# Kernel optimization log

Measured on AMD Instinct MI355X. Metric: run time of the kernel, lower is better.

Reference implementation:

```python
import jax, jax.numpy as jnp
import numpy as np

B, L, Z, G = 512, 2713, 58, 8  # batch, chem features, seq len (zeta), d_model (gamma)
H, HD, FF, NL = 8, 1, 2048, 6  # heads, head_dim, ffn dim, layers
RNA_IN, LIN1, LIN2 = 1018, 256, 64
CAT, C1, C2 = LIN2 + Z * G, 64, 8  # 528, 64, 8


def setup_inputs() -> dict:
    key = jax.random.key(0)
    ks = iter(jax.random.split(key, 40))
    r = lambda shape, s=0.05: (jax.random.normal(next(ks), shape, dtype=jnp.float32) * s)
    inp = {
        'rna': jax.random.normal(next(ks), (B, RNA_IN), dtype=jnp.float32),
        'drug': jax.random.normal(next(ks), (B, L, Z), dtype=jnp.float32),
        'lin1_w': r((LIN1, RNA_IN)), 'lin1_b': r((LIN1,)),
        'lin2_w': r((LIN2, LIN1)), 'lin2_b': r((LIN2,)),
        'chem_w': r((G, L)),  # chem_embedding: Linear(2713->8, no bias)
        'pos_w': r((G, Z)),   # pos_embedding on one-hot == its weight columns
        'qkv_w': r((NL, 3 * G, G)), 'qkv_b': r((NL, 3 * G)),
        'out_w': r((NL, G, G)), 'out_b': r((NL, G)),
        'ln1_g': jnp.ones((NL, G), jnp.float32), 'ln1_b': jnp.zeros((NL, G), jnp.float32),
        'ff1_w': r((NL, FF, G)), 'ff1_b': r((NL, FF)),
        'ff2_w': r((NL, G, FF)), 'ff2_b': r((NL, G)),
        'ln2_g': jnp.ones((NL, G), jnp.float32), 'ln2_b': jnp.zeros((NL, G), jnp.float32),
        'c1_w': r((C1, CAT)), 'c1_b': r((C1,)),
        'c2_w': r((C2, C1)), 'c2_b': r((C2,)),
        'c3_w': r((1, C2)), 'c3_b': r((1,)),
    }
    return inp


def _layernorm(x, g, b, eps=1e-5):
    mu = jnp.mean(x, axis=-1, keepdims=True)
    var = jnp.mean(jnp.square(x - mu), axis=-1, keepdims=True)
    return (x - mu) * jax.lax.rsqrt(var + eps) * g + b


def _forward(rna, drug, lin1_w, lin1_b, lin2_w, lin2_b, chem_w, pos_w,
             qkv_w, qkv_b, out_w, out_b, ln1_g, ln1_b,
             ff1_w, ff1_b, ff2_w, ff2_b, ln2_g, ln2_b,
             c1_w, c1_b, c2_w, c2_b, c3_w, c3_b):
    # rna branch: two linear layers (no activation in original forward)
    r = rna @ lin1_w.T + lin1_b
    r = r @ lin2_w.T + lin2_b  # [B, 64]

    # Embedding: E = W_chem @ M + W_pos (the double loop, vectorized)
    E = jnp.einsum('gl,blz->bgz', chem_w, drug) + pos_w[None]  # [B, G, Z]
    x = jnp.transpose(E, (0, 2, 1))  # [B, Z, G] (batch_first transformer input)

    scale = 1.0 / np.sqrt(HD)
    for i in range(NL):  # 6 post-norm TransformerEncoderLayers, relu FFN
        qkv = x @ qkv_w[i].T + qkv_b[i]  # [B, Z, 3G]
        q, k, v = jnp.split(qkv, 3, axis=-1)
        qh = q.reshape(B, Z, H, HD)
        kh = k.reshape(B, Z, H, HD)
        vh = v.reshape(B, Z, H, HD)
        scores = jnp.einsum('bshd,bthd->bhst', qh, kh) * scale
        a = jax.nn.softmax(scores, axis=-1)
        o = jnp.einsum('bhst,bthd->bshd', a, vh).reshape(B, Z, G)
        o = o @ out_w[i].T + out_b[i]
        x = _layernorm(x + o, ln1_g[i], ln1_b[i])
        ff = jax.nn.relu(x @ ff1_w[i].T + ff1_b[i]) @ ff2_w[i].T + ff2_b[i]
        x = _layernorm(x + ff, ln2_g[i], ln2_b[i])

    flat = x.reshape(B, Z * G)  # [B, 464]
    h = jnp.concatenate([r, flat], axis=1)  # [B, 528]
    h = h @ c1_w.T + c1_b
    h = h @ c2_w.T + c2_b
    return h @ c3_w.T + c3_b  # [B, 1]


def reference(rna, drug, lin1_w, lin1_b, lin2_w, lin2_b, chem_w, pos_w,
              qkv_w, qkv_b, out_w, out_b, ln1_g, ln1_b,
              ff1_w, ff1_b, ff2_w, ff2_b, ln2_g, ln2_b,
              c1_w, c1_b, c2_w, c2_b, c3_w, c3_b):
    return _forward(rna, drug, lin1_w, lin1_b, lin2_w, lin2_b, chem_w, pos_w,
                    qkv_w, qkv_b, out_w, out_b, ln1_g, ln1_b,
                    ff1_w, ff1_b, ff2_w, ff2_b, ln2_g, ln2_b,
                    c1_w, c1_b, c2_w, c2_b, c3_w, c3_b)
```

## Files before the change

### kernel.cpp

```cpp
#include <hip/hip_runtime.h>

#define BB 512
#define LDIM 2713
#define ZDIM 58
#define GDIM 8
#define NLAYER 6
#define FFDIM 2048
#define RNAIN 1018
#define CATDIM 528
#define NCAT 1482
#define LQ 679

typedef float v2f __attribute__((ext_vector_type(2)));
typedef float f32x4 __attribute__((ext_vector_type(4)));
typedef _Float16 f16x4 __attribute__((ext_vector_type(4)));

#define OFF_WCATT  0
#define OFF_BPRIME 94848

__global__ __launch_bounds__(1024) void prep_kernel(
    const float* __restrict__ lin1_w, const float* __restrict__ lin1_b,
    const float* __restrict__ lin2_w, const float* __restrict__ lin2_b,
    const float* __restrict__ c1_w, const float* __restrict__ c1_b,
    float* __restrict__ ws) {
    __shared__ float lin1s[256 * 64];
    __shared__ float Ut[64 * 64];
    __shared__ float c1T[64 * 64];
    const int t = threadIdx.x;
    float* WcatT = ws + OFF_WCATT;

    if (blockIdx.x == 16) {
        {
            int m = t >> 4, q = t & 15;
            float a = 0.f;
            #pragma unroll
            for (int nn = 0; nn < 16; ++nn)
                a += lin2_w[m * 256 + q * 16 + nn] * lin1_b[q * 16 + nn];
            lin1s[m * 16 + q] = a;
        }
        __syncthreads();
        if (t < 64) {
            float a = lin2_b[t];
            #pragma unroll
            for (int q = 0; q < 16; ++q) a += lin1s[t * 16 + q];
            Ut[t] = a;
        }
        __syncthreads();
        if (t < 64) {
            float a = c1_b[t];
            #pragma unroll 8
            for (int m = 0; m < 64; ++m) a += c1_w[t * CATDIM + m] * Ut[m];
            ws[OFF_BPRIME + t] = a;
        }
        for (int i = t; i < 464 * 64; i += 1024) {
            int j = i / 464, kk = i % 464;
            WcatT[(RNAIN + kk) * 64 + j] = c1_w[j * CATDIM + 64 + kk];
        }
        return;
    }

    const int k0 = blockIdx.x * 64;
    const int nk = (RNAIN - k0 < 64) ? (RNAIN - k0) : 64;
    for (int i = t; i < 256 * 64; i += 1024) {
        int n = i >> 6, kl = i & 63;
        lin1s[i] = (kl < nk) ? lin1_w[n * RNAIN + k0 + kl] : 0.f;
    }
    for (int i = t; i < 64 * 64; i += 1024) {
        int j = i >> 6, m = i & 63;
        c1T[m * 64 + j] = c1_w[j * CATDIM + m];
    }
    __syncthreads();
    for (int mp = 0; mp < 4; ++mp) {
        int m = (t >> 6) + mp * 16;
        int kl = t & 63;
        const float* l2r = lin2_w + m * 256;
        float a = 0.f;
        #pragma unroll 8
        for (int n = 0; n < 256; ++n) a += l2r[n] * lin1s[n * 64 + kl];
        Ut[m * 64 + kl] = a;
    }
    __syncthreads();
    for (int kp = 0; kp < 4; ++kp) {
        int kr = (t >> 6) + kp * 16;
        int j = t & 63;
        if (kr < nk) {
            float a = 0.f;
            #pragma unroll 8
            for (int m = 0; m < 64; ++m) a += Ut[m * 64 + kr] * c1T[m * 64 + j];
            WcatT[(k0 + kr) * 64 + j] = a;
        }
    }
}

__global__ __launch_bounds__(512, 8) void mega_kernel(
    const float* __restrict__ drug, const float* __restrict__ chem_w,
    const float* __restrict__ pos_w,
    const float* __restrict__ ff1_w, const float* __restrict__ ff2_w,
    const float* __restrict__ ff1_b,
    const float* __restrict__ qkv_w, const float* __restrict__ qkv_b,
    const float* __restrict__ out_w, const float* __restrict__ out_b,
    const float* __restrict__ ln1_g, const float* __restrict__ ln1_b,
    const float* __restrict__ ff2_b,
    const float* __restrict__ ln2_g, const float* __restrict__ ln2_b,
    const float* __restrict__ rna, const float* __restrict__ WcatT,
    const float* __restrict__ bprime,
    const float* __restrict__ c2_w, const float* __restrict__ c2_b,
    const float* __restrict__ c3_w, const float* __restrict__ c3_b,
    float* __restrict__ out) {
    __shared__ float smem[9152];
    float* cwl    = smem;
    float* part_e = smem + 5440;
    float* xs    = smem;
    float* qs    = smem + 512;
    float* ks    = smem + 992;
    float* vs    = smem + 1472;
    float* part  = smem + 1952;
    float* qkvws = smem + 6048;
    float* qkvbs = smem + 7200;
    float* outws = smem + 7344;
    float* outbs = smem + 7728;
    float* l1gs  = smem + 7776;
    float* l1bs  = smem + 7824;
    float* l2gs  = smem + 7872;
    float* l2bs  = smem + 7920;
    float* f2bs  = smem + 7968;
    float* h1s   = smem + 8016;
    float* h2s   = smem + 8080;

    const int b = blockIdx.x;
    const int t = threadIdx.x;
    const int w = __builtin_amdgcn_readfirstlane(t >> 6);
    const int lane = t & 63;
    const int quad = lane >> 4;
    const int i16 = lane & 15;

    {
        const int zc = (lane < ZDIM) ? lane : (ZDIM - 1);
        v2f acc0 = {0.f, 0.f}, acc1 = {0.f, 0.f}, acc2 = {0.f, 0.f}, acc3 = {0.f, 0.f};
        for (int q = 0; q < 4; ++q) {
            const int l0 = q * LQ;
            const int nrows = (LDIM - l0 < LQ) ? (LDIM - l0) : LQ;
            __syncthreads();
            #pragma unroll
            for (int g = 0; g < 8; ++g)
                for (int i = t; i < nrows; i += 512)
                    cwl[i * 8 + g] = chem_w[g * LDIM + l0 + i];
            __syncthreads();
            const float* dp = drug + (size_t)b * (LDIM * ZDIM) + (size_t)l0 * ZDIM;
            int r0 = w * 85;
            int r1 = (r0 + 85 < nrows) ? (r0 + 85) : nrows;
            int r = r0;
            for (; r + 4 <= r1; r += 4) {
                float d0 = dp[(r + 0) * ZDIM + zc];
                float d1 = dp[(r + 1) * ZDIM + zc];
                float d2 = dp[(r + 2) * ZDIM + zc];
                float d3 = dp[(r + 3) * ZDIM + zc];
                const v2f* c0 = (const v2f*)(cwl + (r + 0) * 8);
                const v2f* c1 = (const v2f*)(cwl + (r + 1) * 8);
                const v2f* c2 = (const v2f*)(cwl + (r + 2) * 8);
                const v2f* c3 = (const v2f*)(cwl + (r + 3) * 8);
                v2f dd;
                dd = (v2f){d0, d0};
                acc0 += c0[0] * dd; acc1 += c0[1] * dd; acc2 += c0[2] * dd; acc3 += c0[3] * dd;
                dd = (v2f){d1, d1};
                acc0 += c1[0] * dd; acc1 += c1[1] * dd; acc2 += c1[2] * dd; acc3 += c1[3] * dd;
                dd = (v2f){d2, d2};
                acc0 += c2[0] * dd; acc1 += c2[1] * dd; acc2 += c2[2] * dd; acc3 += c2[3] * dd;
                dd = (v2f){d3, d3};
                acc0 += c3[0] * dd; acc1 += c3[1] * dd; acc2 += c3[2] * dd; acc3 += c3[3] * dd;
            }
            for (; r < r1; ++r) {
                float d = dp[r * ZDIM + zc];
                const v2f* cc = (const v2f*)(cwl + r * 8);
                v2f dd = {d, d};
                acc0 += cc[0] * dd; acc1 += cc[1] * dd; acc2 += cc[2] * dd; acc3 += cc[3] * dd;
            }
        }
        if (lane < ZDIM) {
            v2f* pr = (v2f*)(part_e + w * 464 + zc * 8);
            pr[0] = acc0; pr[1] = acc1; pr[2] = acc2; pr[3] = acc3;
        }
        __syncthreads();
        if (t < 464) {
            int z = t >> 3, g = t & 7;
            float s = pos_w[g * ZDIM + z];
            #pragma unroll
            for (int ww = 0; ww < 8; ++ww) s += part_e[ww * 464 + t];
            xs[t] = s;
        } else if (t < 512) {
            xs[t] = 0.f;
        }
        __syncthreads();
    }

    for (int i = t; i < 1152; i += 512) qkvws[i] = qkv_w[i];
    if (t < 144) qkvbs[t] = qkv_b[t];
    if (t < 384) outws[t] = out_w[t];
    if (t < 48) {
        outbs[t] = out_b[t];
        l1gs[t] = ln1_g[t]; l1bs[t] = ln1_b[t];
        l2gs[t] = ln2_g[t]; l2bs[t] = ln2_b[t];
        f2bs[t] = ff2_b[t];
    }
    __syncthreads();

    for (int li = 0; li < NLAYER; ++li) {
        if (t < 464) {
            int z = t >> 3, h = t & 7;
            const float4* xr = (const float4*)(xs + z * 8);
            float4 x0 = xr[0], x1 = xr[1];
            #pragma unroll
            for (int p = 0; p < 3; ++p) {
                int j = p * 8 + h;
                const float4* wr = (const float4*)(qkvws + li * 192 + j * 8);
                float4 w0 = wr[0], w1 = wr[1];
                float a = qkvbs[li * 24 + j]
                        + x0.x * w0.x + x0.y * w0.y + x0.z * w0.z + x0.w * w0.w
                        + x1.x * w1.x + x1.y * w1.y + x1.z * w1.z + x1.w * w1.w;
                float* dst = (p == 0) ? qs : (p == 1) ? ks : vs;
                dst[h * 60 + z] = a;
            }
        }
        __syncthreads();

        if (t < 464) {
            int h = t & 7, s = t >> 3;
            float q = qs[h * 60 + s];
            const float4* kr = (const float4*)(ks + h * 60);
            const float4* vr = (const float4*)(vs + h * 60);
            float sum = 0.f, oa = 0.f;
            #pragma unroll 2
            for (int c = 0; c < 14; ++c) {
                float4 k4 = kr[c], v4 = vr[c];
                float e0 = __expf(q * k4.x); sum += e0; oa += e0 * v4.x;
                float e1 = __expf(q * k4.y); sum += e1; oa += e1 * v4.y;
                float e2 = __expf(q * k4.z); sum += e2; oa += e2 * v4.z;
                float e3 = __expf(q * k4.w); sum += e3; oa += e3 * v4.w;
            }
            {
                const float* kk = ks + h * 60;
                const float* vv = vs + h * 60;
                float e0 = __expf(q * kk[56]); sum += e0; oa += e0 * vv[56];
                float e1 = __expf(q * kk[57]); sum += e1; oa += e1 * vv[57];
            }
            float o = oa / sum;
            int g = h;
            float a = outbs[li * 8 + g] + xs[t];
            const float* wr8 = outws + li * 64 + g * 8;
            #pragma unroll
            for (int hh = 0; hh < 8; ++hh)
                a += __shfl(o, hh, 8) * wr8[hh];
            float s8 = a + __shfl_xor(a, 1);
            s8 += __shfl_xor(s8, 2);
            s8 += __shfl_xor(s8, 4);
            float mu = s8 * 0.125f;
            float d = a - mu;
            float vv = d * d;
            vv += __shfl_xor(vv, 1); vv += __shfl_xor(vv, 2); vv += __shfl_xor(vv, 4);
            float inv = rsqrtf(vv * 0.125f + 1e-5f);
            xs[t] = d * inv * l1gs[li * 8 + g] + l1bs[li * 8 + g];
        }
        __syncthreads();

        {
            f16x4 xb[4];
            #pragma unroll
            for (int nt = 0; nt < 4; ++nt) {
                if (quad < 2) {
                    const float4* xp = (const float4*)(xs + (nt * 16 + i16) * 8 + quad * 4);
                    float4 xv = *xp;
                    xb[nt][0] = (_Float16)xv.x; xb[nt][1] = (_Float16)xv.y;
                    xb[nt][2] = (_Float16)xv.z; xb[nt][3] = (_Float16)xv.w;
                } else {
                    xb[nt][0] = (_Float16)0.f; xb[nt][1] = (_Float16)0.f;
                    xb[nt][2] = (_Float16)0.f; xb[nt][3] = (_Float16)0.f;
                }
            }
            f32x4 oacc[4];
            #pragma unroll
            for (int nt = 0; nt < 4; ++nt) { oacc[nt][0]=0.f; oacc[nt][1]=0.f; oacc[nt][2]=0.f; oacc[nt][3]=0.f; }

            const float* w1p = ff1_w + ((size_t)li * FFDIM + w * 256) * 8;
            const float* a2p = ff2_w + (size_t)li * GDIM * FFDIM + w * 256;
            const float* b1p = ff1_b + li * FFDIM + w * 256;

            #pragma unroll 2
            for (int ft = 0; ft < 16; ++ft) {
                f16x4 w1f = {};
                if (lane < 32) {
                    f32x4 v = *(const f32x4*)(w1p + (size_t)(ft * 16 + i16) * 8 + quad * 4);
                    w1f[0] = (_Float16)v[0]; w1f[1] = (_Float16)v[1];
                    w1f[2] = (_Float16)v[2]; w1f[3] = (_Float16)v[3];
                }
                f16x4 a2f = {};
                if (i16 < 8) {
                    f32x4 v = *(const f32x4*)(a2p + (size_t)i16 * FFDIM + ft * 16 + quad * 4);
                    a2f[0] = (_Float16)v[0]; a2f[1] = (_Float16)v[1];
                    a2f[2] = (_Float16)v[2]; a2f[3] = (_Float16)v[3];
                }
                f32x4 b1v = *(const f32x4*)(b1p + ft * 16 + quad * 4);
                #pragma unroll
                for (int nt = 0; nt < 4; ++nt) {
                    f32x4 h = b1v;
                    h = __builtin_amdgcn_mfma_f32_16x16x16f16(w1f, xb[nt], h, 0, 0, 0);
                    h[0] = fmaxf(h[0], 0.f); h[1] = fmaxf(h[1], 0.f);
                    h[2] = fmaxf(h[2], 0.f); h[3] = fmaxf(h[3], 0.f);
                    f16x4 hb;
                    hb[0] = (_Float16)h[0]; hb[1] = (_Float16)h[1];
                    hb[2] = (_Float16)h[2]; hb[3] = (_Float16)h[3];
                    oacc[nt] = __builtin_amdgcn_mfma_f32_16x16x16f16(a2f, hb, oacc[nt], 0, 0, 0);
                }
            }
            if (quad < 2) {
                #pragma unroll
                for (int nt = 0; nt < 4; ++nt) {
                    float4 o4 = make_float4(oacc[nt][0], oacc[nt][1], oacc[nt][2], oacc[nt][3]);
                    *(float4*)(part + ((w * 64 + nt * 16 + i16) * 8 + quad * 4)) = o4;
                }
            }
        }
        __syncthreads();

        if (t < 464) {
            int z = t >> 3, g = t & 7;
            float s = 0.f;
            #pragma unroll
            for (int ww = 0; ww < 8; ++ww) s += part[(ww * 64 + z) * 8 + g];
            float a = xs[t] + s + f2bs[li * 8 + g];
            float s8 = a + __shfl_xor(a, 1);
            s8 += __shfl_xor(s8, 2);
            s8 += __shfl_xor(s8, 4);
            float mu = s8 * 0.125f;
            float d = a - mu;
            float vv = d * d;
            vv += __shfl_xor(vv, 1); vv += __shfl_xor(vv, 2); vv += __shfl_xor(vv, 4);
            float inv = rsqrtf(vv * 0.125f + 1e-5f);
            xs[t] = d * inv * l2gs[li * 8 + g] + l2bs[li * 8 + g];
        }
        __syncthreads();
    }

    {
        float* cat = part;
        float* partial = part + 1024;
        const float* rg = rna + (size_t)b * RNAIN;
        for (int i = t; i < RNAIN; i += 512) cat[i] = rg[i];
        __syncthreads();
        int j = lane;
        int k0 = w * 186;
        int k1 = (k0 + 186 < NCAT) ? (k0 + 186) : NCAT;
        float a = (w == 0) ? bprime[j] : 0.f;
        #pragma unroll 4
        for (int k = k0; k < k1; ++k) {
            float ck = (k < RNAIN) ? cat[k] : xs[k - RNAIN];
            a += ck * WcatT[k * 64 + j];
        }
        partial[w * 64 + j] = a;
        __syncthreads();
        if (t < 64) {
            float s = 0.f;
            #pragma unroll
            for (int ww = 0; ww < 8; ++ww) s += partial[ww * 64 + t];
            h1s[t] = s;
        }
    }
    __syncthreads();
    if (t < 8) {
        float a2 = c2_b[t];
        #pragma unroll 8
        for (int m = 0; m < 64; ++m) a2 += h1s[m] * c2_w[t * 64 + m];
        h2s[t] = a2;
    }
    __syncthreads();
    if (t == 0) {
        float a3 = c3_b[0];
        #pragma unroll
        for (int jj = 0; jj < 8; ++jj) a3 += h2s[jj] * c3_w[jj];
        out[b] = a3;
    }
}

extern "C" void kernel_launch(void* const* d_in, const int* in_sizes, int n_in,
                              void* d_out, int out_size, void* d_ws, size_t ws_size,
                              hipStream_t stream) {
    const float* rna    = (const float*)d_in[0];
    const float* drug   = (const float*)d_in[1];
    const float* lin1_w = (const float*)d_in[2];
    const float* lin1_b = (const float*)d_in[3];
    const float* lin2_w = (const float*)d_in[4];
    const float* lin2_b = (const float*)d_in[5];
    const float* chem_w = (const float*)d_in[6];
    const float* pos_w  = (const float*)d_in[7];
    const float* qkv_w  = (const float*)d_in[8];
    const float* qkv_b  = (const float*)d_in[9];
    const float* out_w  = (const float*)d_in[10];
    const float* out_b  = (const float*)d_in[11];
    const float* ln1_g  = (const float*)d_in[12];
    const float* ln1_b  = (const float*)d_in[13];
    const float* ff1_w  = (const float*)d_in[14];
    const float* ff1_b  = (const float*)d_in[15];
    const float* ff2_w  = (const float*)d_in[16];
    const float* ff2_b  = (const float*)d_in[17];
    const float* ln2_g  = (const float*)d_in[18];
    const float* ln2_b  = (const float*)d_in[19];
    const float* c1_w   = (const float*)d_in[20];
    const float* c1_b   = (const float*)d_in[21];
    const float* c2_w   = (const float*)d_in[22];
    const float* c2_b   = (const float*)d_in[23];
    const float* c3_w   = (const float*)d_in[24];
    const float* c3_b   = (const float*)d_in[25];
    float* ws  = (float*)d_ws;
    float* out = (float*)d_out;

    hipLaunchKernelGGL(prep_kernel, dim3(17), dim3(1024), 0, stream,
                       lin1_w, lin1_b, lin2_w, lin2_b, c1_w, c1_b, ws);
    hipLaunchKernelGGL(mega_kernel, dim3(BB), dim3(512), 0, stream,
                       drug, chem_w, pos_w, ff1_w, ff2_w, ff1_b,
                       qkv_w, qkv_b, out_w, out_b,
                       ln1_g, ln1_b, ff2_b, ln2_g, ln2_b,
                       rna, ws + OFF_WCATT, ws + OFF_BPRIME,
                       c2_w, c2_b, c3_w, c3_b, out);
}
```

Before: 698.9 us.

## Double mega_kernel block size, pre-pack FFN weights to fp16, restructure prep GEMMs

Measured after the change: 650.7 us. -6.9%, faster.

```diff
diff --git a/kernel.cpp b/kernel.cpp
--- a/kernel.cpp
+++ b/kernel.cpp
@@ -17,19 +17,49 @@
 
 #define OFF_WCATT  0
 #define OFF_BPRIME 94848
+#define OFF_W1H    94912
+#define OFF_A2H    144064
 
 __global__ __launch_bounds__(1024) void prep_kernel(
     const float* __restrict__ lin1_w, const float* __restrict__ lin1_b,
     const float* __restrict__ lin2_w, const float* __restrict__ lin2_b,
     const float* __restrict__ c1_w, const float* __restrict__ c1_b,
+    const float* __restrict__ ff1_w, const float* __restrict__ ff2_w,
     float* __restrict__ ws) {
+    const int t = threadIdx.x;
+    const int bx = blockIdx.x;
+    float* WcatT = ws + OFF_WCATT;
+
+    if (bx >= 17) {
+        int tid = (bx - 17) * 1024 + t;
+        _Float16* w1hp = (_Float16*)(ws + OFF_W1H);
+        _Float16* a2hp = (_Float16*)(ws + OFF_A2H);
+        if (tid < NLAYER * 128 * 32) {
+            int li = tid / 4096, rem = tid % 4096;
+            int ft = rem >> 5, l32 = rem & 31;
+            int q = l32 >> 4, i = l32 & 15;
+            const float* src = ff1_w + ((size_t)li * FFDIM + ft * 16 + i) * 8 + q * 4;
+            size_t dst = ((size_t)(li * 128 + ft) * 32 + l32) * 4;
+            #pragma unroll
+            for (int j = 0; j < 4; ++j) w1hp[dst + j] = (_Float16)src[j];
+        } else {
+            int r2 = tid - NLAYER * 128 * 32;
+            int li = r2 / 4096, rem = r2 % 4096;
+            int ft = rem >> 5, s = rem & 31;
+            int q = s >> 3, i2 = s & 7;
+            const float* src = ff2_w + ((size_t)li * GDIM + i2) * FFDIM + ft * 16 + q * 4;
+            size_t dst = ((size_t)(li * 128 + ft) * 32 + s) * 4;
+            #pragma unroll
+            for (int j = 0; j < 4; ++j) a2hp[dst + j] = (_Float16)src[j];
+        }
+        return;
+    }
+
     __shared__ float lin1s[256 * 64];
     __shared__ float Ut[64 * 64];
     __shared__ float c1T[64 * 64];
-    const int t = threadIdx.x;
-    float* WcatT = ws + OFF_WCATT;
-
-    if (blockIdx.x == 16) {
+
+    if (bx == 16) {
         {
             int m = t >> 4, q = t & 15;
             float a = 0.f;
@@ -59,7 +89,7 @@
         return;
     }
 
-    const int k0 = blockIdx.x * 64;
+    const int k0 = bx * 64;
     const int nk = (RNAIN - k0 < 64) ? (RNAIN - k0) : 64;
     for (int i = t; i < 256 * 64; i += 1024) {
         int n = i >> 6, kl = i & 63;
@@ -70,32 +100,45 @@
         c1T[m * 64 + j] = c1_w[j * CATDIM + m];
     }
     __syncthreads();
-    for (int mp = 0; mp < 4; ++mp) {
-        int m = (t >> 6) + mp * 16;
-        int kl = t & 63;
-        const float* l2r = lin2_w + m * 256;
-        float a = 0.f;
-        #pragma unroll 8
-        for (int n = 0; n < 256; ++n) a += l2r[n] * lin1s[n * 64 + kl];
-        Ut[m * 64 + kl] = a;
+    {
+        const int kl = t & 63;
+        const int mw = __builtin_amdgcn_readfirstlane(t >> 6);
+        float a0 = 0.f, a1 = 0.f, a2 = 0.f, a3 = 0.f;
+        for (int n = 0; n < 256; ++n) {
+            float ls = lin1s[n * 64 + kl];
+            a0 += lin2_w[(mw +  0) * 256 + n] * ls;
+            a1 += lin2_w[(mw + 16) * 256 + n] * ls;
+            a2 += lin2_w[(mw + 32) * 256 + n] * ls;
+            a3 += lin2_w[(mw + 48) * 256 + n] * ls;
+        }
+        Ut[(mw +  0) * 64 + kl] = a0;
+        Ut[(mw + 16) * 64 + kl] = a1;
+        Ut[(mw + 32) * 64 + kl] = a2;
+        Ut[(mw + 48) * 64 + kl] = a3;
     }
     __syncthreads();
-    for (int kp = 0; kp < 4; ++kp) {
-        int kr = (t >> 6) + kp * 16;
-        int j = t & 63;
-        if (kr < nk) {
-            float a = 0.f;
-            #pragma unroll 8
-            for (int m = 0; m < 64; ++m) a += Ut[m * 64 + kr] * c1T[m * 64 + j];
-            WcatT[(k0 + kr) * 64 + j] = a;
-        }
+    {
+        const int j = t & 63;
+        const int kw = __builtin_amdgcn_readfirstlane(t >> 6);
+        float a0 = 0.f, a1 = 0.f, a2 = 0.f, a3 = 0.f;
+        for (int m = 0; m < 64; ++m) {
+            float cv = c1T[m * 64 + j];
+            a0 += Ut[m * 64 + kw +  0] * cv;
+            a1 += Ut[m * 64 + kw + 16] * cv;
+            a2 += Ut[m * 64 + kw + 32] * cv;
+            a3 += Ut[m * 64 + kw + 48] * cv;
+        }
+        if (kw +  0 < nk) WcatT[(k0 + kw +  0) * 64 + j] = a0;
+        if (kw + 16 < nk) WcatT[(k0 + kw + 16) * 64 + j] = a1;
+        if (kw + 32 < nk) WcatT[(k0 + kw + 32) * 64 + j] = a2;
+        if (kw + 48 < nk) WcatT[(k0 + kw + 48) * 64 + j] = a3;
     }
 }
 
-__global__ __launch_bounds__(512, 8) void mega_kernel(
+__global__ __launch_bounds__(1024, 8) void mega_kernel(
     const float* __restrict__ drug, const float* __restrict__ chem_w,
     const float* __restrict__ pos_w,
-    const float* __restrict__ ff1_w, const float* __restrict__ ff2_w,
+    const _Float16* __restrict__ w1h, const _Float16* __restrict__ a2h,
     const float* __restrict__ ff1_b,
     const float* __restrict__ qkv_w, const float* __restrict__ qkv_b,
     const float* __restrict__ out_w, const float* __restrict__ out_b,
@@ -107,25 +150,26 @@
     const float* __restrict__ c2_w, const float* __restrict__ c2_b,
     const float* __restrict__ c3_w, const float* __restrict__ c3_b,
     float* __restrict__ out) {
-    __shared__ float smem[9152];
+    __shared__ float smem[12864];
     float* cwl    = smem;
     float* part_e = smem + 5440;
     float* xs    = smem;
-    float* qs    = smem + 512;
-    float* ks    = smem + 992;
-    float* vs    = smem + 1472;
-    float* part  = smem + 1952;
-    float* qkvws = smem + 6048;
-    float* qkvbs = smem + 7200;
-    float* outws = smem + 7344;
-    float* outbs = smem + 7728;
-    float* l1gs  = smem + 7776;
-    float* l1bs  = smem + 7824;
-    float* l2gs  = smem + 7872;
-    float* l2bs  = smem + 7920;
-    float* f2bs  = smem + 7968;
-    float* h1s   = smem + 8016;
-    float* h2s   = smem + 8080;
+    _Float16* xh = (_Float16*)(smem + 512);
+    float* qs    = smem + 768;
+    float* ks    = smem + 1248;
+    float* vs    = smem + 1728;
+    float* part  = smem + 2208;
+    float* qkvws = smem + 10400;
+    float* qkvbs = smem + 11552;
+    float* outws = smem + 11696;
+    float* outbs = smem + 12080;
+    float* l1gs  = smem + 12128;
+    float* l1bs  = smem + 12176;
+    float* l2gs  = smem + 12224;
+    float* l2bs  = smem + 12272;
+    float* f2bs  = smem + 12320;
+    float* h1s   = smem + 12368;
+    float* h2s   = smem + 12432;
 
     const int b = blockIdx.x;
     const int t = threadIdx.x;
@@ -142,38 +186,45 @@
             const int nrows = (LDIM - l0 < LQ) ? (LDIM - l0) : LQ;
             __syncthreads();
             #pragma unroll
-            for (int g = 0; g < 8; ++g)
-                for (int i = t; i < nrows; i += 512)
-                    cwl[i * 8 + g] = chem_w[g * LDIM + l0 + i];
+            for (int gp = 0; gp < 4; ++gp)
+                for (int i = t; i < nrows; i += 1024) {
+                    v2f cv = { chem_w[(2 * gp) * LDIM + l0 + i],
+                               chem_w[(2 * gp + 1) * LDIM + l0 + i] };
+                    *(v2f*)(cwl + 2 * (gp * 680 + i)) = cv;
+                }
             __syncthreads();
-            const float* dp = drug + (size_t)b * (LDIM * ZDIM) + (size_t)l0 * ZDIM;
-            int r0 = w * 85;
-            int r1 = (r0 + 85 < nrows) ? (r0 + 85) : nrows;
+            const float* dp = drug + (size_t)b * (LDIM * ZDIM) + (size_t)l0 * ZDIM + zc;
+            int r0 = w * 43;
+            int r1 = (r0 + 43 < nrows) ? (r0 + 43) : nrows;
             int r = r0;
-            for (; r + 4 <= r1; r += 4) {
-                float d0 = dp[(r + 0) * ZDIM + zc];
-                float d1 = dp[(r + 1) * ZDIM + zc];
-                float d2 = dp[(r + 2) * ZDIM + zc];
-                float d3 = dp[(r + 3) * ZDIM + zc];
-                const v2f* c0 = (const v2f*)(cwl + (r + 0) * 8);
-                const v2f* c1 = (const v2f*)(cwl + (r + 1) * 8);
-                const v2f* c2 = (const v2f*)(cwl + (r + 2) * 8);
-                const v2f* c3 = (const v2f*)(cwl + (r + 3) * 8);
-                v2f dd;
-                dd = (v2f){d0, d0};
-                acc0 += c0[0] * dd; acc1 += c0[1] * dd; acc2 += c0[2] * dd; acc3 += c0[3] * dd;
-                dd = (v2f){d1, d1};
-                acc0 += c1[0] * dd; acc1 += c1[1] * dd; acc2 += c1[2] * dd; acc3 += c1[3] * dd;
-                dd = (v2f){d2, d2};
-                acc0 += c2[0] * dd; acc1 += c2[1] * dd; acc2 += c2[2] * dd; acc3 += c2[3] * dd;
-                dd = (v2f){d3, d3};
-                acc0 += c3[0] * dd; acc1 += c3[1] * dd; acc2 += c3[2] * dd; acc3 += c3[3] * dd;
+            for (; r + 8 <= r1; r += 8) {
+                float d0 = dp[(r + 0) * ZDIM];
+                float d1 = dp[(r + 1) * ZDIM];
+                float d2 = dp[(r + 2) * ZDIM];
+                float d3 = dp[(r + 3) * ZDIM];
+                float d4 = dp[(r + 4) * ZDIM];
+                float d5 = dp[(r + 5) * ZDIM];
+                float d6 = dp[(r + 6) * ZDIM];
+                float d7 = dp[(r + 7) * ZDIM];
+                #pragma unroll
+                for (int j = 0; j < 8; ++j) {
+                    float dj = (j == 0) ? d0 : (j == 1) ? d1 : (j == 2) ? d2 : (j == 3) ? d3
+                             : (j == 4) ? d4 : (j == 5) ? d5 : (j == 6) ? d6 : d7;
+                    v2f dd = {dj, dj};
+                    int rr = r + j;
+                    acc0 += *(const v2f*)(cwl + 2 * (0 * 680 + rr)) * dd;
+                    acc1 += *(const v2f*)(cwl + 2 * (1 * 680 + rr)) * dd;
+                    acc2 += *(const v2f*)(cwl + 2 * (2 * 680 + rr)) * dd;
+                    acc3 += *(const v2f*)(cwl + 2 * (3 * 680 + rr)) * dd;
+                }
             }
             for (; r < r1; ++r) {
-                float d = dp[r * ZDIM + zc];
-                const v2f* cc = (const v2f*)(cwl + r * 8);
+                float d = dp[r * ZDIM];
                 v2f dd = {d, d};
-                acc0 += cc[0] * dd; acc1 += cc[1] * dd; acc2 += cc[2] * dd; acc3 += cc[3] * dd;
+                acc0 += *(const v2f*)(cwl + 2 * (0 * 680 + r)) * dd;
+                acc1 += *(const v2f*)(cwl + 2 * (1 * 680 + r)) * dd;
+                acc2 += *(const v2f*)(cwl + 2 * (2 * 680 + r)) * dd;
+                acc3 += *(const v2f*)(cwl + 2 * (3 * 680 + r)) * dd;
             }
         }
         if (lane < ZDIM) {
@@ -185,15 +236,16 @@
             int z = t >> 3, g = t & 7;
             float s = pos_w[g * ZDIM + z];
             #pragma unroll
-            for (int ww = 0; ww < 8; ++ww) s += part_e[ww * 464 + t];
+            for (int ww = 0; ww < 16; ++ww) s += part_e[ww * 464 + t];
             xs[t] = s;
         } else if (t < 512) {
             xs[t] = 0.f;
-        }
-        __syncthreads();
-    }
-
-    for (int i = t; i < 1152; i += 512) qkvws[i] = qkv_w[i];
+            xh[t] = (_Float16)0.f;
+        }
+        __syncthreads();
+    }
+
+    for (int i = t; i < 1152; i += 1024) qkvws[i] = qkv_w[i];
     if (t < 144) qkvbs[t] = qkv_b[t];
     if (t < 384) outws[t] = out_w[t];
     if (t < 48) {
@@ -205,21 +257,18 @@
     __syncthreads();
 
     for (int li = 0; li < NLAYER; ++li) {
-        if (t < 464) {
-            int z = t >> 3, h = t & 7;
+        for (int i = t; i < 1392; i += 1024) {
+            int z = i / 24, j = i - z * 24;
             const float4* xr = (const float4*)(xs + z * 8);
             float4 x0 = xr[0], x1 = xr[1];
-            #pragma unroll
-            for (int p = 0; p < 3; ++p) {
-                int j = p * 8 + h;
-                const float4* wr = (const float4*)(qkvws + li * 192 + j * 8);
-                float4 w0 = wr[0], w1 = wr[1];
-                float a = qkvbs[li * 24 + j]
-                        + x0.x * w0.x + x0.y * w0.y + x0.z * w0.z + x0.w * w0.w
-                        + x1.x * w1.x + x1.y * w1.y + x1.z * w1.z + x1.w * w1.w;
-                float* dst = (p == 0) ? qs : (p == 1) ? ks : vs;
-                dst[h * 60 + z] = a;
-            }
+            const float4* wr = (const float4*)(qkvws + li * 192 + j * 8);
+            float4 w0 = wr[0], w1 = wr[1];
+            float a = qkvbs[li * 24 + j]
+                    + x0.x * w0.x + x0.y * w0.y + x0.z * w0.z + x0.w * w0.w
+                    + x1.x * w1.x + x1.y * w1.y + x1.z * w1.z + x1.w * w1.w;
+            int p = j >> 3, h = j & 7;
+            float* dst = (p == 0) ? qs : (p == 1) ? ks : vs;
+            dst[h * 60 + z] = a;
         }
         __syncthreads();
 
@@ -258,7 +307,9 @@
             float vv = d * d;
             vv += __shfl_xor(vv, 1); vv += __shfl_xor(vv, 2); vv += __shfl_xor(vv, 4);
             float inv = rsqrtf(vv * 0.125f + 1e-5f);
-            xs[t] = d * inv * l1gs[li * 8 + g] + l1bs[li * 8 + g];
+            float xn = d * inv * l1gs[li * 8 + g] + l1bs[li * 8 + g];
+            xs[t] = xn;
+            xh[t] = (_Float16)xn;
         }
         __syncthreads();
 
@@ -267,10 +318,7 @@
             #pragma unroll
             for (int nt = 0; nt < 4; ++nt) {
                 if (quad < 2) {
-                    const float4* xp = (const float4*)(xs + (nt * 16 + i16) * 8 + quad * 4);
-                    float4 xv = *xp;
-                    xb[nt][0] = (_Float16)xv.x; xb[nt][1] = (_Float16)xv.y;
-                    xb[nt][2] = (_Float16)xv.z; xb[nt][3] = (_Float16)xv.w;
+                    xb[nt] = *(const f16x4*)(xh + (nt * 16 + i16) * 8 + quad * 4);
                 } else {
                     xb[nt][0] = (_Float16)0.f; xb[nt][1] = (_Float16)0.f;
                     xb[nt][2] = (_Float16)0.f; xb[nt][3] = (_Float16)0.f;
@@ -280,29 +328,20 @@
             #pragma unroll
             for (int nt = 0; nt < 4; ++nt) { oacc[nt][0]=0.f; oacc[nt][1]=0.f; oacc[nt][2]=0.f; oacc[nt][3]=0.f; }
 
-            const float* w1p = ff1_w + ((size_t)li * FFDIM + w * 256) * 8;
-            const float* a2p = ff2_w + (size_t)li * GDIM * FFDIM + w * 256;
-            const float* b1p = ff1_b + li * FFDIM + w * 256;
-
-            #pragma unroll 2
-            for (int ft = 0; ft < 16; ++ft) {
+            const _Float16* w1p = w1h + ((size_t)(li * 128 + w * 8) * 32) * 4;
+            const _Float16* a2p = a2h + ((size_t)(li * 128 + w * 8) * 32) * 4;
+            const float* b1p = ff1_b + li * FFDIM + w * 128;
+
+            #pragma unroll
+            for (int ft = 0; ft < 8; ++ft) {
                 f16x4 w1f = {};
-                if (lane < 32) {
-                    f32x4 v = *(const f32x4*)(w1p + (size_t)(ft * 16 + i16) * 8 + quad * 4);
-                    w1f[0] = (_Float16)v[0]; w1f[1] = (_Float16)v[1];
-                    w1f[2] = (_Float16)v[2]; w1f[3] = (_Float16)v[3];
-                }
+                if (lane < 32) w1f = *(const f16x4*)(w1p + (size_t)(ft * 32 + lane) * 4);
                 f16x4 a2f = {};
-                if (i16 < 8) {
-                    f32x4 v = *(const f32x4*)(a2p + (size_t)i16 * FFDIM + ft * 16 + quad * 4);
-                    a2f[0] = (_Float16)v[0]; a2f[1] = (_Float16)v[1];
-                    a2f[2] = (_Float16)v[2]; a2f[3] = (_Float16)v[3];
-                }
+                if (i16 < 8) a2f = *(const f16x4*)(a2p + (size_t)(ft * 32 + quad * 8 + i16) * 4);
                 f32x4 b1v = *(const f32x4*)(b1p + ft * 16 + quad * 4);
                 #pragma unroll
                 for (int nt = 0; nt < 4; ++nt) {
-                    f32x4 h = b1v;
-                    h = __builtin_amdgcn_mfma_f32_16x16x16f16(w1f, xb[nt], h, 0, 0, 0);
+                    f32x4 h = __builtin_amdgcn_mfma_f32_16x16x16f16(w1f, xb[nt], b1v, 0, 0, 0);
                     h[0] = fmaxf(h[0], 0.f); h[1] = fmaxf(h[1], 0.f);
                     h[2] = fmaxf(h[2], 0.f); h[3] = fmaxf(h[3], 0.f);
                     f16x4 hb;
@@ -325,7 +364,7 @@
             int z = t >> 3, g = t & 7;
             float s = 0.f;
             #pragma unroll
-            for (int ww = 0; ww < 8; ++ww) s += part[(ww * 64 + z) * 8 + g];
+            for (int ww = 0; ww < 16; ++ww) s += part[(ww * 64 + z) * 8 + g];
             float a = xs[t] + s + f2bs[li * 8 + g];
             float s8 = a + __shfl_xor(a, 1);
             s8 += __shfl_xor(s8, 2);
@@ -342,13 +381,13 @@
 
     {
         float* cat = part;
-        float* partial = part + 1024;
+        float* partial = part + 2048;
         const float* rg = rna + (size_t)b * RNAIN;
-        for (int i = t; i < RNAIN; i += 512) cat[i] = rg[i];
+        for (int i = t; i < RNAIN; i += 1024) cat[i] = rg[i];
         __syncthreads();
         int j = lane;
-        int k0 = w * 186;
-        int k1 = (k0 + 186 < NCAT) ? (k0 + 186) : NCAT;
+        int k0 = w * 93;
+        int k1 = (k0 + 93 < NCAT) ? (k0 + 93) : NCAT;
         float a = (w == 0) ? bprime[j] : 0.f;
         #pragma unroll 4
         for (int k = k0; k < k1; ++k) {
@@ -360,7 +399,7 @@
         if (t < 64) {
             float s = 0.f;
             #pragma unroll
-            for (int ww = 0; ww < 8; ++ww) s += partial[ww * 64 + t];
+            for (int ww = 0; ww < 16; ++ww) s += partial[ww * 64 + t];
             h1s[t] = s;
         }
     }
@@ -412,11 +451,12 @@
     float* ws  = (float*)d_ws;
     float* out = (float*)d_out;
 
-    hipLaunchKernelGGL(prep_kernel, dim3(17), dim3(1024), 0, stream,
-                       lin1_w, lin1_b, lin2_w, lin2_b, c1_w, c1_b, ws);
-    hipLaunchKernelGGL(mega_kernel, dim3(BB), dim3(512), 0, stream,
-                       drug, chem_w, pos_w, ff1_w, ff2_w, ff1_b,
-                       qkv_w, qkv_b, out_w, out_b,
+    hipLaunchKernelGGL(prep_kernel, dim3(65), dim3(1024), 0, stream,
+                       lin1_w, lin1_b, lin2_w, lin2_b, c1_w, c1_b, ff1_w, ff2_w, ws);
+    hipLaunchKernelGGL(mega_kernel, dim3(BB), dim3(1024), 0, stream,
+                       drug, chem_w, pos_w,
+                       (const _Float16*)(ws + OFF_W1H), (const _Float16*)(ws + OFF_A2H),
+                       ff1_b, qkv_w, qkv_b, out_w, out_b,
                        ln1_g, ln1_b, ff2_b, ln2_g, ln2_b,
                        rna, ws + OFF_WCATT, ws + OFF_BPRIME,
                        c2_w, c2_b, c3_w, c3_b, out);
```
